# Optimization experiments

Hardware: AMD Instinct MI355X
Metric: run time of the kernel (lower is better)

The kernel has to match this reference:

```python
import jax, jax.numpy as jnp
import numpy as np

# Tiny fixed contraction dims: M=3^(r_1-k), K=3^k, N=3^(r_2-k) with r_1=r_2=2, k=1
M, K, N = 3, 3, 3
R_O = 2  # output tensor rank -> output trailing shape (3,)*R_O == (3,3)


def setup_inputs() -> dict:
    key = jax.random.key(0)
    k1, k2 = jax.random.split(key)
    P, B, C = 4, 8192, 128
    T1 = jax.random.normal(k1, (P, B, C, M, K), dtype=jnp.float32)
    T2 = jax.random.normal(k2, (1, B, C, K, N), dtype=jnp.float32)
    return {"T1": T1, "T2": T2}


def reference(T1, T2):
    P, B, C = T1.shape[:3]
    T1m = T1.reshape(P, B, C, M, K)
    # T2 has a broadcast path dim of size 1; drop it and broadcast via einsum
    T2m = T2.reshape(B, C, K, N)
    out = jnp.einsum('pbcik,bckj->pbcij', T1m, T2m)
    return out.reshape((P, B, C) + (3,) * R_O)
```

## Files before the change

### kernel.cpp

```cpp
#include <hip/hip_runtime.h>


typedef float floatx4 __attribute__((ext_vector_type(4)));

__global__ __launch_bounds__(256) void tc33_kernel(const float* __restrict__ T1,
                                                   const float* __restrict__ T2,
                                                   float* __restrict__ out) {
    __shared__ float sA[2304];
    __shared__ float sB[2304];
    const long long PER_P = 9LL * 8192 * 128;
    const int tid = threadIdx.x;
    const long long base = (long long)blockIdx.x * 2304;

    floatx4* SA4 = reinterpret_cast<floatx4*>(sA);
    floatx4* SB4 = reinterpret_cast<floatx4*>(sB);

    {
        const floatx4* Bg = reinterpret_cast<const floatx4*>(T2 + base);
        const floatx4* Ag = reinterpret_cast<const floatx4*>(T1 + base);
        floatx4 rb0 = Bg[tid], rb1 = Bg[tid + 256];
        floatx4 ra0 = Ag[tid], ra1 = Ag[tid + 256];
        SB4[tid] = rb0; SB4[tid + 256] = rb1;
        SA4[tid] = ra0; SA4[tid + 256] = ra1;
        if (tid < 64) {
            floatx4 rb2 = Bg[tid + 512];
            floatx4 ra2 = Ag[tid + 512];
            SB4[tid + 512] = rb2;
            SA4[tid + 512] = ra2;
        }
    }
    __syncthreads();

    float b[9];
    #pragma unroll
    for (int i = 0; i < 9; ++i) b[i] = sB[tid * 9 + i];

    #pragma unroll
    for (int p = 0; p < 4; ++p) {
        float a[9];
        #pragma unroll
        for (int i = 0; i < 9; ++i) a[i] = sA[tid * 9 + i];

        float o[9];
        #pragma unroll
        for (int i = 0; i < 3; ++i) {
            #pragma unroll
            for (int j = 0; j < 3; ++j) {
                float s = a[i * 3 + 0] * b[0 * 3 + j];
                s = fmaf(a[i * 3 + 1], b[1 * 3 + j], s);
                s = fmaf(a[i * 3 + 2], b[2 * 3 + j], s);
                o[i * 3 + j] = s;
            }
        }

        #pragma unroll
        for (int i = 0; i < 9; ++i) sB[tid * 9 + i] = o[i];

        __syncthreads();

        floatx4 na0, na1, na2;
        if (p < 3) {
            const floatx4* An =
                reinterpret_cast<const floatx4*>(T1 + (p + 1) * PER_P + base);
            na0 = An[tid];
            na1 = An[tid + 256];
            if (tid < 64) na2 = An[tid + 512];
        }

        {
            floatx4* O4 = reinterpret_cast<floatx4*>(out + p * PER_P + base);
            const floatx4* S4 = reinterpret_cast<const floatx4*>(sB);
            __builtin_nontemporal_store(S4[tid      ], &O4[tid      ]);
            __builtin_nontemporal_store(S4[tid + 256], &O4[tid + 256]);
            if (tid < 64)
                __builtin_nontemporal_store(S4[tid + 512], &O4[tid + 512]);
        }

        if (p < 3) {
            SA4[tid      ] = na0;
            SA4[tid + 256] = na1;
            if (tid < 64) SA4[tid + 512] = na2;
        }

        __syncthreads();
    }
}

extern "C" void kernel_launch(void* const* d_in, const int* in_sizes, int n_in,
                              void* d_out, int out_size, void* d_ws, size_t ws_size,
                              hipStream_t stream) {
    const float* T1 = (const float*)d_in[0];
    const float* T2 = (const float*)d_in[1];
    float* out = (float*)d_out;

    const int threads = 256;
    const int blocks = (8192 * 128) / 256;
    tc33_kernel<<<blocks, threads, 0, stream>>>(T1, T2, out);
}
```

Measured before the change: 285.3 us.

## Load inputs directly per thread and stage outputs through per-wave LDS slices

Each thread now loads its own 3x3 T1 and T2 matrices straight from global memory into registers with strided vector loads, and prefetches the next path's T1 into registers. Shared memory is used only to transpose outputs, split into per-wave slices, so block-wide __syncthreads are replaced by wave barriers. This removes input staging through LDS and the block-level synchronisation. The cost is uncoalesced, strided 36-byte-per-thread global loads instead of fully coalesced block loads.

```diff
diff --git a/kernel.cpp b/kernel.cpp
--- a/kernel.cpp
+++ b/kernel.cpp
@@ -6,40 +6,45 @@
 __global__ __launch_bounds__(256) void tc33_kernel(const float* __restrict__ T1,
                                                    const float* __restrict__ T2,
                                                    float* __restrict__ out) {
-    __shared__ float sA[2304];
-    __shared__ float sB[2304];
+    __shared__ float so[2304];
     const long long PER_P = 9LL * 8192 * 128;
     const int tid = threadIdx.x;
-    const long long base = (long long)blockIdx.x * 2304;
+    const int w = tid >> 6;
+    const int l = tid & 63;
+    const long long cell  = (long long)blockIdx.x * 256 + tid;
+    const long long cbase = cell * 9;
+    const long long wbase = (long long)blockIdx.x * 2304 + (long long)w * 576;
 
-    floatx4* SA4 = reinterpret_cast<floatx4*>(sA);
-    floatx4* SB4 = reinterpret_cast<floatx4*>(sB);
-
-    {
-        const floatx4* Bg = reinterpret_cast<const floatx4*>(T2 + base);
-        const floatx4* Ag = reinterpret_cast<const floatx4*>(T1 + base);
-        floatx4 rb0 = Bg[tid], rb1 = Bg[tid + 256];
-        floatx4 ra0 = Ag[tid], ra1 = Ag[tid + 256];
-        SB4[tid] = rb0; SB4[tid + 256] = rb1;
-        SA4[tid] = ra0; SA4[tid + 256] = ra1;
-        if (tid < 64) {
-            floatx4 rb2 = Bg[tid + 512];
-            floatx4 ra2 = Ag[tid + 512];
-            SB4[tid + 512] = rb2;
-            SA4[tid + 512] = ra2;
-        }
-    }
-    __syncthreads();
+    float* slice = so + w * 576;
+    floatx4* S4  = reinterpret_cast<floatx4*>(slice);
 
     float b[9];
-    #pragma unroll
-    for (int i = 0; i < 9; ++i) b[i] = sB[tid * 9 + i];
+    {
+        floatx4 v0 = *reinterpret_cast<const floatx4*>(T2 + cbase);
+        floatx4 v1 = *reinterpret_cast<const floatx4*>(T2 + cbase + 4);
+        float   v8 = T2[cbase + 8];
+        b[0] = v0.x; b[1] = v0.y; b[2] = v0.z; b[3] = v0.w;
+        b[4] = v1.x; b[5] = v1.y; b[6] = v1.z; b[7] = v1.w;
+        b[8] = v8;
+    }
+
+    floatx4 ra0 = *reinterpret_cast<const floatx4*>(T1 + cbase);
+    floatx4 ra1 = *reinterpret_cast<const floatx4*>(T1 + cbase + 4);
+    float   ra8 = T1[cbase + 8];
 
     #pragma unroll
     for (int p = 0; p < 4; ++p) {
         float a[9];
-        #pragma unroll
-        for (int i = 0; i < 9; ++i) a[i] = sA[tid * 9 + i];
+        a[0] = ra0.x; a[1] = ra0.y; a[2] = ra0.z; a[3] = ra0.w;
+        a[4] = ra1.x; a[5] = ra1.y; a[6] = ra1.z; a[7] = ra1.w;
+        a[8] = ra8;
+
+        if (p < 3) {
+            const float* An = T1 + (long long)(p + 1) * PER_P + cbase;
+            ra0 = *reinterpret_cast<const floatx4*>(An);
+            ra1 = *reinterpret_cast<const floatx4*>(An + 4);
+            ra8 = An[8];
+        }
 
         float o[9];
         #pragma unroll
@@ -54,35 +59,21 @@
         }
 
         #pragma unroll
-        for (int i = 0; i < 9; ++i) sB[tid * 9 + i] = o[i];
+        for (int i = 0; i < 9; ++i) slice[l * 9 + i] = o[i];
 
-        __syncthreads();
+        __builtin_amdgcn_wave_barrier();
 
-        floatx4 na0, na1, na2;
-        if (p < 3) {
-            const floatx4* An =
-                reinterpret_cast<const floatx4*>(T1 + (p + 1) * PER_P + base);
-            na0 = An[tid];
-            na1 = An[tid + 256];
-            if (tid < 64) na2 = An[tid + 512];
-        }
+        floatx4 s0 = S4[l];
+        floatx4 s1 = S4[l + 64];
+        floatx4 s2;
+        if (l < 16) s2 = S4[l + 128];
 
-        {
-            floatx4* O4 = reinterpret_cast<floatx4*>(out + p * PER_P + base);
-            const floatx4* S4 = reinterpret_cast<const floatx4*>(sB);
-            __builtin_nontemporal_store(S4[tid      ], &O4[tid      ]);
-            __builtin_nontemporal_store(S4[tid + 256], &O4[tid + 256]);
-            if (tid < 64)
-                __builtin_nontemporal_store(S4[tid + 512], &O4[tid + 512]);
-        }
+        floatx4* O4 = reinterpret_cast<floatx4*>(out + (long long)p * PER_P + wbase);
+        __builtin_nontemporal_store(s0, &O4[l]);
+        __builtin_nontemporal_store(s1, &O4[l + 64]);
+        if (l < 16) __builtin_nontemporal_store(s2, &O4[l + 128]);
 
-        if (p < 3) {
-            SA4[tid      ] = na0;
-            SA4[tid + 256] = na1;
-            if (tid < 64) SA4[tid + 512] = na2;
-        }
-
-        __syncthreads();
+        __builtin_amdgcn_wave_barrier();
     }
 }
 
```

After: 283.0 us. About the same (-0.8%).
